# Kernel tuning notes

Measured on AMD Instinct MI355X. Metric: run time of the kernel, lower is better.

The kernel has to match this reference:

```python
import jax, jax.numpy as jnp
import numpy as np

OFF_DIAGONAL_SCALE = 1.0


def setup_inputs() -> dict:
    key = jax.random.key(0)
    k1, k2 = jax.random.split(key)
    B, V, T, H, W = 32, 8, 2, 192, 288
    y_true = jax.random.normal(k1, (B, V, T, H, W), dtype=jnp.float32)
    # y_pred near y_true so the residual covariance is well-conditioned
    y_pred = y_true + 0.1 * jax.random.normal(k2, (B, V, T, H, W), dtype=jnp.float32)
    return {"y_true": y_true, "y_pred": y_pred}


def reference(y_true, y_pred):
    # (batch, var, time, lat, lon) -> (var, time, batch, lat, lon) -> (D, N)
    B, V, T, H, W = y_true.shape
    D, N = V * T, B * H * W
    yt2d = jnp.transpose(y_true, (1, 2, 0, 3, 4)).reshape(D, N)
    yp2d = jnp.transpose(y_pred, (1, 2, 0, 3, 4)).reshape(D, N)
    residual = yt2d - yp2d                                  # (D, N)

    # torch.cov: rows = variables, unbiased (N-1) normalization
    centered = residual - jnp.mean(residual, axis=1, keepdims=True)
    cov = (centered @ centered.T) / (N - 1)                 # (D, D)
    precision = jnp.linalg.inv(cov)

    eye = jnp.eye(D, dtype=precision.dtype)
    precision = precision * (1.0 - eye) * OFF_DIAGONAL_SCALE + precision * eye

    # per-point Mahalanobis quadratic form r_n^T P r_n, fused as one batched contraction
    quad = jnp.einsum('dn,de,en->n', residual, precision, residual)  # (N,)
    return jnp.mean(quad)  # reduction='mean'
```

## Files before the change

### kernel.cpp

```cpp
#include <hip/hip_runtime.h>

#define D        16
#define NPAIR    136
#define NVALS    152
#define HW       55296
#define BSTRIDE  884736
#define NTOT     1769472
#define CPB      6912
#define BPP      8
#define G        256
#define TCOLS    256
#define TPB      27
#define NBUF     4
#define TSTR     260

typedef __attribute__((ext_vector_type(8))) short short8;
typedef __attribute__((ext_vector_type(4))) float f32x4;

__device__ __forceinline__ float wave_reduce(float x) {
    x += __shfl_down(x, 32);
    x += __shfl_down(x, 16);
    x += __shfl_down(x, 8);
    x += __shfl_down(x, 4);
    x += __shfl_down(x, 2);
    x += __shfl_down(x, 1);
    return x;
}

__host__ __device__ constexpr int tri_idx(int d, int e) {
    return d * D - (d * (d - 1)) / 2 + (e - d);
}

__device__ __forceinline__ short f2bf(float x) {
    union { float f; unsigned u; } v; v.f = x;
    const unsigned r = (v.u + 0x7fffu + ((v.u >> 16) & 1u)) >> 16;
    return (short)r;
}

__global__ __launch_bounds__(256)
void gram_mfma(const float* __restrict__ yt, const float* __restrict__ yp,
               float* __restrict__ part) {
    __shared__ __align__(16) float tile[NBUF][2][D][TSTR];

    const int tid  = threadIdx.x;
    const int lane = tid & 63;
    const int wid  = tid >> 6;
    const int b    = blockIdx.x / BPP;
    const int hw0  = (blockIdx.x - b * BPP) * CPB;
    const float* bt = yt + (size_t)b * BSTRIDE + hw0;
    const float* bp = yp + (size_t)b * BSTRIDE + hw0;

    const int row = lane & 15;
    const int kg  = lane >> 4;

    f32x4 acc = {0.0f, 0.0f, 0.0f, 0.0f};
    float rs = 0.0f;

    auto stage = [&](int tt, int bb) {
#pragma unroll
        for (int s = 0; s < 4; ++s) {
            const int r = s * 4 + wid;
            const float* gt = bt + (size_t)r * HW + tt * TCOLS + lane * 4;
            const float* gq = bp + (size_t)r * HW + tt * TCOLS + lane * 4;
            __builtin_amdgcn_global_load_lds(
                (const __attribute__((address_space(1))) void*)gt,
                (__attribute__((address_space(3))) void*)&tile[bb][0][r][0],
                16, 0, 0);
            __builtin_amdgcn_global_load_lds(
                (const __attribute__((address_space(1))) void*)gq,
                (__attribute__((address_space(3))) void*)&tile[bb][1][r][0],
                16, 0, 0);
        }
    };

    auto compute = [&](int bb) {
#pragma unroll
        for (int c = 0; c < 2; ++c) {
            const int base = wid * 64 + c * 32 + kg * 8;
            const float* pt = &tile[bb][0][row][base];
            const float* pq = &tile[bb][1][row][base];
            const float r0 = pt[0] - pq[0], r1 = pt[1] - pq[1];
            const float r2 = pt[2] - pq[2], r3 = pt[3] - pq[3];
            const float r4 = pt[4] - pq[4], r5 = pt[5] - pq[5];
            const float r6 = pt[6] - pq[6], r7 = pt[7] - pq[7];
            rs += ((r0 + r1) + (r2 + r3)) + ((r4 + r5) + (r6 + r7));
            short8 f;
            f[0] = f2bf(r0); f[1] = f2bf(r1); f[2] = f2bf(r2); f[3] = f2bf(r3);
            f[4] = f2bf(r4); f[5] = f2bf(r5); f[6] = f2bf(r6); f[7] = f2bf(r7);
            acc = __builtin_amdgcn_mfma_f32_16x16x32_bf16(f, f, acc, 0, 0, 0);
        }
    };

    stage(0, 0);
    stage(1, 1);
    stage(2, 2);
#pragma unroll 4
    for (int t = 0; t < TPB - 3; ++t) {
        asm volatile("s_waitcnt vmcnt(16)" ::: "memory");
        __builtin_amdgcn_s_barrier();
        stage(t + 3, (t + 3) & 3);
        compute(t & 3);
    }
    asm volatile("s_waitcnt vmcnt(16)" ::: "memory");
    __builtin_amdgcn_s_barrier();
    compute((TPB - 3) & 3);
    asm volatile("s_waitcnt vmcnt(8)" ::: "memory");
    __builtin_amdgcn_s_barrier();
    compute((TPB - 2) & 3);
    asm volatile("s_waitcnt vmcnt(0)" ::: "memory");
    __builtin_amdgcn_s_barrier();
    compute((TPB - 1) & 3);

    rs += __shfl_xor(rs, 16);
    rs += __shfl_xor(rs, 32);

    __shared__ float cpart[4][D][D];
    __shared__ float spart[4][D];
    __syncthreads();
#pragma unroll
    for (int i = 0; i < 4; ++i)
        cpart[wid][kg * 4 + i][row] = acc[i];
    if (lane < D) spart[wid][lane] = rs;
    __syncthreads();

    const int d = tid >> 4, e = tid & 15;
    if (d <= e) {
        const float s = (cpart[0][d][e] + cpart[1][d][e]) +
                        (cpart[2][d][e] + cpart[3][d][e]);
        part[tri_idx(d, e) * G + blockIdx.x] = s;
    }
    if (tid < D) {
        const float s = (spart[0][tid] + spart[1][tid]) +
                        (spart[2][tid] + spart[3][tid]);
        part[(NPAIR + tid) * G + blockIdx.x] = s;
    }
}

__global__ void reduce_part(const float* __restrict__ part,
                            float* __restrict__ S) {
    const int vi   = blockIdx.x;
    const int tid  = threadIdx.x;
    const int lane = tid & 63;
    const int wv   = tid >> 6;
    float s = 0.0f;
    for (int j = tid; j < G; j += 256) s += part[vi * G + j];
    s = wave_reduce(s);
    __shared__ float ws[4];
    if (lane == 0) ws[wv] = s;
    __syncthreads();
    if (tid == 0) S[vi] = (ws[0] + ws[1]) + (ws[2] + ws[3]);
}

__global__ void finalize_kernel(const float* __restrict__ S,
                                float* __restrict__ out) {
    __shared__ float Stri[NPAIR];
    __shared__ float Ssum[D];
    __shared__ float A[D][2 * D + 1];

    const int tid  = threadIdx.x;
    const int lane = tid & 63;
    const int wv   = tid >> 6;

    if (tid < NVALS) {
        const float v = S[tid];
        if (tid < NPAIR) Stri[tid]         = v;
        else             Ssum[tid - NPAIR] = v;
    }
    __syncthreads();

    {
        const int d = tid >> 4, e = tid & 15;
        const int lo = d < e ? d : e, hi = d < e ? e : d;
        const float invN = 1.0f / (float)NTOT;
        const float cov = (Stri[tri_idx(lo, hi)] -
                           Ssum[d] * Ssum[e] * invN) /
                          (float)(NTOT - 1);
        A[d][e]     = cov;
        A[d][D + e] = (d == e) ? 1.0f : 0.0f;
    }
    __syncthreads();

    const int r0 = tid >> 5;
    const int c0 = tid & 31;
    const int r1 = r0 + 8;
    for (int k = 0; k < D; ++k) {
        const float pivinv = 1.0f / A[k][k];
        __syncthreads();
        if (tid < 32) A[k][tid] *= pivinv;
        __syncthreads();
        const float f0 = A[r0][k];
        const float f1 = A[r1][k];
        __syncthreads();
        const float akc = A[k][c0];
        if (r0 != k) A[r0][c0] -= f0 * akc;
        if (r1 != k) A[r1][c0] -= f1 * akc;
        __syncthreads();
    }

    float term;
    {
        const int d = tid >> 4, e = tid & 15;
        const int lo = d < e ? d : e, hi = d < e ? e : d;
        float p = A[d][D + e];
        const float scale = 1.0f;
        if (d != e) p *= scale;
        term = p * Stri[tri_idx(lo, hi)];
    }
    term = wave_reduce(term);

    __shared__ float wsum[4];
    if (lane == 0) wsum[wv] = term;
    __syncthreads();
    if (tid == 0) {
        const float tot = (wsum[0] + wsum[1]) + (wsum[2] + wsum[3]);
        out[0] = tot / (float)NTOT;
    }
}

extern "C" void kernel_launch(void* const* d_in, const int* in_sizes, int n_in,
                              void* d_out, int out_size, void* d_ws, size_t ws_size,
                              hipStream_t stream) {
    const float* y_true = (const float*)d_in[0];
    const float* y_pred = (const float*)d_in[1];
    float* out  = (float*)d_out;
    float* part = (float*)d_ws;
    float* S    = part + (size_t)NVALS * G;

    hipLaunchKernelGGL(gram_mfma, dim3(G), dim3(256), 0, stream,
                       y_true, y_pred, part);
    hipLaunchKernelGGL(reduce_part, dim3(NVALS), dim3(256), 0, stream,
                       part, S);
    hipLaunchKernelGGL(finalize_kernel, dim3(1), dim3(256), 0, stream,
                       S, out);
}
```

Measured before the change: 45.44 us.

## Double gram kernel waves to 512 threads and fold partial reduction into finalize

The Gram-matrix kernel now runs 8 waves per block instead of 4. Each wave stages half as many rows and does one MFMA per tile instead of two, and the vmcnt waits are rescaled to match. The separate reduce_part launch is removed: the single-block finalize kernel now sums the 256 per-block partials for all 152 values itself. This is meant to add latency hiding in the bandwidth-bound stage and save a kernel launch, at the cost of a serial reduction inside one block.

```diff
diff --git a/kernel.cpp b/kernel.cpp
--- a/kernel.cpp
+++ b/kernel.cpp
@@ -37,7 +37,7 @@
     return (short)r;
 }
 
-__global__ __launch_bounds__(256)
+__global__ __launch_bounds__(512)
 void gram_mfma(const float* __restrict__ yt, const float* __restrict__ yp,
                float* __restrict__ part) {
     __shared__ __align__(16) float tile[NBUF][2][D][TSTR];
@@ -58,8 +58,8 @@
 
     auto stage = [&](int tt, int bb) {
 #pragma unroll
-        for (int s = 0; s < 4; ++s) {
-            const int r = s * 4 + wid;
+        for (int s = 0; s < 2; ++s) {
+            const int r = s * 8 + wid;
             const float* gt = bt + (size_t)r * HW + tt * TCOLS + lane * 4;
             const float* gq = bp + (size_t)r * HW + tt * TCOLS + lane * 4;
             __builtin_amdgcn_global_load_lds(
@@ -74,21 +74,18 @@
     };
 
     auto compute = [&](int bb) {
-#pragma unroll
-        for (int c = 0; c < 2; ++c) {
-            const int base = wid * 64 + c * 32 + kg * 8;
-            const float* pt = &tile[bb][0][row][base];
-            const float* pq = &tile[bb][1][row][base];
-            const float r0 = pt[0] - pq[0], r1 = pt[1] - pq[1];
-            const float r2 = pt[2] - pq[2], r3 = pt[3] - pq[3];
-            const float r4 = pt[4] - pq[4], r5 = pt[5] - pq[5];
-            const float r6 = pt[6] - pq[6], r7 = pt[7] - pq[7];
-            rs += ((r0 + r1) + (r2 + r3)) + ((r4 + r5) + (r6 + r7));
-            short8 f;
-            f[0] = f2bf(r0); f[1] = f2bf(r1); f[2] = f2bf(r2); f[3] = f2bf(r3);
-            f[4] = f2bf(r4); f[5] = f2bf(r5); f[6] = f2bf(r6); f[7] = f2bf(r7);
-            acc = __builtin_amdgcn_mfma_f32_16x16x32_bf16(f, f, acc, 0, 0, 0);
-        }
+        const int base = wid * 32 + kg * 8;
+        const float* pt = &tile[bb][0][row][base];
+        const float* pq = &tile[bb][1][row][base];
+        const float r0 = pt[0] - pq[0], r1 = pt[1] - pq[1];
+        const float r2 = pt[2] - pq[2], r3 = pt[3] - pq[3];
+        const float r4 = pt[4] - pq[4], r5 = pt[5] - pq[5];
+        const float r6 = pt[6] - pq[6], r7 = pt[7] - pq[7];
+        rs += ((r0 + r1) + (r2 + r3)) + ((r4 + r5) + (r6 + r7));
+        short8 f;
+        f[0] = f2bf(r0); f[1] = f2bf(r1); f[2] = f2bf(r2); f[3] = f2bf(r3);
+        f[4] = f2bf(r4); f[5] = f2bf(r5); f[6] = f2bf(r6); f[7] = f2bf(r7);
+        acc = __builtin_amdgcn_mfma_f32_16x16x32_bf16(f, f, acc, 0, 0, 0);
     };
 
     stage(0, 0);
@@ -96,15 +93,15 @@
     stage(2, 2);
 #pragma unroll 4
     for (int t = 0; t < TPB - 3; ++t) {
-        asm volatile("s_waitcnt vmcnt(16)" ::: "memory");
+        asm volatile("s_waitcnt vmcnt(8)" ::: "memory");
         __builtin_amdgcn_s_barrier();
         stage(t + 3, (t + 3) & 3);
         compute(t & 3);
     }
-    asm volatile("s_waitcnt vmcnt(16)" ::: "memory");
+    asm volatile("s_waitcnt vmcnt(8)" ::: "memory");
     __builtin_amdgcn_s_barrier();
     compute((TPB - 3) & 3);
-    asm volatile("s_waitcnt vmcnt(8)" ::: "memory");
+    asm volatile("s_waitcnt vmcnt(4)" ::: "memory");
     __builtin_amdgcn_s_barrier();
     compute((TPB - 2) & 3);
     asm volatile("s_waitcnt vmcnt(0)" ::: "memory");
@@ -114,8 +111,8 @@
     rs += __shfl_xor(rs, 16);
     rs += __shfl_xor(rs, 32);
 
-    __shared__ float cpart[4][D][D];
-    __shared__ float spart[4][D];
+    __shared__ float cpart[8][D][D];
+    __shared__ float spart[8][D];
     __syncthreads();
 #pragma unroll
     for (int i = 0; i < 4; ++i)
@@ -123,35 +120,24 @@
     if (lane < D) spart[wid][lane] = rs;
     __syncthreads();
 
-    const int d = tid >> 4, e = tid & 15;
-    if (d <= e) {
-        const float s = (cpart[0][d][e] + cpart[1][d][e]) +
-                        (cpart[2][d][e] + cpart[3][d][e]);
-        part[tri_idx(d, e) * G + blockIdx.x] = s;
-    }
-    if (tid < D) {
-        const float s = (spart[0][tid] + spart[1][tid]) +
-                        (spart[2][tid] + spart[3][tid]);
-        part[(NPAIR + tid) * G + blockIdx.x] = s;
-    }
-}
-
-__global__ void reduce_part(const float* __restrict__ part,
-                            float* __restrict__ S) {
-    const int vi   = blockIdx.x;
-    const int tid  = threadIdx.x;
-    const int lane = tid & 63;
-    const int wv   = tid >> 6;
-    float s = 0.0f;
-    for (int j = tid; j < G; j += 256) s += part[vi * G + j];
-    s = wave_reduce(s);
-    __shared__ float ws[4];
-    if (lane == 0) ws[wv] = s;
-    __syncthreads();
-    if (tid == 0) S[vi] = (ws[0] + ws[1]) + (ws[2] + ws[3]);
-}
-
-__global__ void finalize_kernel(const float* __restrict__ S,
+    if (tid < 256) {
+        const int d = tid >> 4, e = tid & 15;
+        if (d <= e) {
+            float s = 0.0f;
+#pragma unroll
+            for (int w = 0; w < 8; ++w) s += cpart[w][d][e];
+            part[tri_idx(d, e) * G + blockIdx.x] = s;
+        }
+        if (tid < D) {
+            float s = 0.0f;
+#pragma unroll
+            for (int w = 0; w < 8; ++w) s += spart[w][tid];
+            part[(NPAIR + tid) * G + blockIdx.x] = s;
+        }
+    }
+}
+
+__global__ void finalize_kernel(const float* __restrict__ part,
                                 float* __restrict__ out) {
     __shared__ float Stri[NPAIR];
     __shared__ float Ssum[D];
@@ -161,10 +147,16 @@
     const int lane = tid & 63;
     const int wv   = tid >> 6;
 
-    if (tid < NVALS) {
-        const float v = S[tid];
-        if (tid < NPAIR) Stri[tid]         = v;
-        else             Ssum[tid - NPAIR] = v;
+    for (int vi = wv; vi < NVALS; vi += 4) {
+        float s = 0.0f;
+#pragma unroll
+        for (int j = 0; j < G / 64; ++j)
+            s += part[vi * G + j * 64 + lane];
+        s = wave_reduce(s);
+        if (lane == 0) {
+            if (vi < NPAIR) Stri[vi]         = s;
+            else            Ssum[vi - NPAIR] = s;
+        }
     }
     __syncthreads();
 
@@ -224,12 +216,9 @@
     const float* y_pred = (const float*)d_in[1];
     float* out  = (float*)d_out;
     float* part = (float*)d_ws;
-    float* S    = part + (size_t)NVALS * G;
-
-    hipLaunchKernelGGL(gram_mfma, dim3(G), dim3(256), 0, stream,
+
+    hipLaunchKernelGGL(gram_mfma, dim3(G), dim3(512), 0, stream,
                        y_true, y_pred, part);
-    hipLaunchKernelGGL(reduce_part, dim3(NVALS), dim3(256), 0, stream,
-                       part, S);
     hipLaunchKernelGGL(finalize_kernel, dim3(1), dim3(256), 0, stream,
-                       S, out);
-}
+                       part, out);
+}
```

Result: slower. 61.05 us (+34.3%).
